# Kernel optimization log

Measured on AMD Instinct MI355X. Metric: run time of the kernel, lower is better.

## Reference

```python
import jax, jax.numpy as jnp
import numpy as np

NU, NI, E = 20000, 8000, 64
DV, DT = 4096, 768
NE, B = 200000, 4096
L_HET, L_HOMO = 2, 1
K_ISG, K_UCG = 10, 20
MMW, WD = 0.1, 1e-4


def setup_inputs() -> dict:
    ks = jax.random.split(jax.random.key(0), 14)
    return {
        "feat_v": jax.random.normal(ks[0], (NI, DV), jnp.float32),
        "feat_t": jax.random.normal(ks[1], (NI, DT), jnp.float32),
        "pref_v": jax.random.normal(ks[2], (NU, E), jnp.float32) * 0.1,
        "pref_t": jax.random.normal(ks[3], (NU, E), jnp.float32) * 0.1,
        "W_v": jax.random.normal(ks[4], (DV, E), jnp.float32) * 0.02,
        "W_t": jax.random.normal(ks[5], (DT, E), jnp.float32) * 0.02,
        "user_v_alpha": jax.random.normal(ks[6], (1,), jnp.float32),
        "user_nb_weights": jax.random.normal(ks[7], (NU, K_UCG), jnp.float32),
        "edge_users": jax.random.randint(ks[8], (NE,), 0, NU, jnp.int32),
        "edge_items": jax.random.randint(ks[9], (NE,), 0, NI, jnp.int32),
        "u_ids": jax.random.randint(ks[10], (B,), 0, NU, jnp.int32),
        "pos_ids": jax.random.randint(ks[11], (B,), 0, NI, jnp.int32),
        "neg_ids": jax.random.randint(ks[12], (B,), 0, NI, jnp.int32),
        "user_nb": jax.random.randint(ks[13], (NU, K_UCG), 0, NU, jnp.int32),
    }


def reference(feat_v, feat_t, pref_v, pref_t, W_v, W_t, user_v_alpha,
              user_nb_weights, edge_users, edge_items, u_ids, pos_ids,
              neg_ids, user_nb):
    N = NU + NI
    # bidirectional bipartite edges (items offset by NU)
    src = jnp.concatenate([edge_users, edge_items + NU])
    dst = jnp.concatenate([edge_items + NU, edge_users])
    deg = jax.ops.segment_sum(jnp.ones_like(src, jnp.float32), dst, num_segments=N)
    deg = jnp.maximum(deg, 1.0)
    norm = (1.0 / jnp.sqrt(deg[src] * deg[dst]))[:, None]

    def hetero_gcn(feat, pref, W):
        x = jnp.concatenate([pref, feat @ W], axis=0)  # [N, E]
        h, out = x, x
        for _ in range(L_HET):
            h = jax.ops.segment_sum(h[src] * norm, dst, num_segments=N)
            out = out + h
        return out[:NU], out[NU:]

    u_v, i_v = hetero_gcn(feat_v, pref_v, W_v)
    u_t, i_t = hetero_gcn(feat_t, pref_t, W_t)
    a_v = jax.nn.sigmoid(user_v_alpha[0])
    u_f = jnp.concatenate([a_v * u_v, (1.0 - a_v) * u_t], axis=1)  # [NU, 2E]
    i_f = jnp.concatenate([i_v, i_t], axis=1)                      # [NI, 2E]

    # Item Semantic Graph: KNN over cosine sim, no grad through adjacency.
    def knn_adj(f):
        fn = f / jnp.linalg.norm(f, axis=-1, keepdims=True)
        sim = fn @ fn.T                       # [NI, NI]
        _, idx = jax.lax.top_k(sim, K_ISG)
        return jnp.zeros((NI, NI), f.dtype).at[jnp.arange(NI)[:, None], idx].set(1.0)

    adj = jax.lax.stop_gradient(MMW * knn_adj(feat_v) + (1.0 - MMW) * knn_adj(feat_t))
    rs = adj.sum(axis=1)
    adj = adj * jnp.where(rs > 0, 1.0 / rs, 0.0)[:, None]

    h_i = i_f
    for _ in range(L_HOMO):
        h_i = adj @ h_i

    # User Co-occurrence Graph: scatter-softmax attention aggregation, vectorized.
    attn = jax.nn.softmax(user_nb_weights, axis=1)  # [NU, K]
    h_u = u_f
    for _ in range(L_HOMO):
        h_u = jnp.einsum('uk,ukd->ud', attn, h_u[user_nb])

    z_u = u_f + h_u
    z_i = i_f + h_i
    pos = jnp.sum(z_u[u_ids] * z_i[pos_ids], axis=1)
    neg = jnp.sum(z_u[u_ids] * z_i[neg_ids], axis=1)
    bpr = -jnp.mean(jax.nn.log_sigmoid(pos - neg))
    reg = WD * (jnp.sum(pref_v ** 2) + jnp.sum(pref_t ** 2) + user_v_alpha[0] ** 2) / 2.0
    return bpr + reg
```

## Files before the change

kernel.cpp:

```cpp
#include <hip/hip_runtime.h>
#include <cstdint>
#include <cstddef>

#define NU_C   20000
#define NI_C   8000
#define NTOT_C 28000
#define NE_C   200000
#define B_C    4096
#define NPAD_C 8064
#define NCHUNK 63
#define NPAIR  2016

typedef unsigned short u16;
typedef unsigned int   u32;
typedef unsigned char  u8;
typedef __bf16 bf16x8 __attribute__((ext_vector_type(8)));
typedef float  f32x4  __attribute__((ext_vector_type(4)));

static __device__ __forceinline__ u16 f2bf(float f) {
  u32 u = __float_as_uint(f);
  return (u16)((u + 0x7fffu + ((u >> 16) & 1u)) >> 16);
}

static __device__ __forceinline__ void gl_lds16(const void* g, void* l) {
  __builtin_amdgcn_global_load_lds(
      (const __attribute__((address_space(1))) void*)g,
      (__attribute__((address_space(3))) void*)l, 16, 0, 0);
}

static __device__ __forceinline__ int xcd_swz(int b) {
  return (b & 7) * (NPAIR / 8) + (b >> 3);
}

static __device__ __forceinline__ void wtrans_body(int b, const float* __restrict__ Wv,
                                                   const float* __restrict__ Wti,
                                                   u16* __restrict__ Ov, u16* __restrict__ Ot) {
  __shared__ u16 sT[64][72];
  const float* W; u16* O; int D;
  if (b < 64) { W = Wv; O = Ov; D = 4096; }
  else        { b -= 64; W = Wti; O = Ot; D = 768; }
  const int k0 = b * 64;
  const int r = threadIdx.x >> 6;
  const int c = threadIdx.x & 63;
  for (int rr = r; rr < 64; rr += 4)
    sT[c][rr] = f2bf(W[(size_t)(k0 + rr) * 64 + c]);
  __syncthreads();
  const int n = threadIdx.x >> 2, seg = threadIdx.x & 3;
  uint4 a0 = *(const uint4*)&sT[n][seg * 16];
  uint4 a1 = *(const uint4*)&sT[n][seg * 16 + 8];
  *(uint4*)(O + (size_t)n * D + k0 + seg * 16)     = a0;
  *(uint4*)(O + (size_t)n * D + k0 + seg * 16 + 8) = a1;
}

__global__ void conv_kernel2(const float* __restrict__ Fv, const float* __restrict__ Ft,
                             u16* __restrict__ Fbv, u16* __restrict__ Fbt,
                             u8* __restrict__ Fv8,
                             float* __restrict__ rnv, float* __restrict__ rnt,
                             const float* __restrict__ pv, const float* __restrict__ pt,
                             float* __restrict__ x2,
                             const float* __restrict__ Wv, const float* __restrict__ Wti,
                             u16* __restrict__ wtv, u16* __restrict__ wtt,
                             const int* __restrict__ eu, const int* __restrict__ ei,
                             float* __restrict__ deg) {
  int b = blockIdx.x;
  const int tid = threadIdx.x;
  float ss = 0.f;
  if (b < NPAD_C) {
    const int row = b;
    u16* dst  = Fbv + (size_t)row * 4096;
    u8*  dst8 = Fv8 + (size_t)row * 4096;
    if (row < NI_C) {
      const float* src = Fv + (size_t)row * 4096;
      for (int c = tid * 4; c < 4096; c += 1024) {
        float4 f = *(const float4*)(src + c);
        ss += f.x*f.x + f.y*f.y + f.z*f.z + f.w*f.w;
        ushort4 v; v.x = f2bf(f.x); v.y = f2bf(f.y); v.z = f2bf(f.z); v.w = f2bf(f.w);
        *(ushort4*)(dst + c) = v;
        int w8 = __builtin_amdgcn_cvt_pk_fp8_f32(f.x, f.y, 0, false);
        w8 = __builtin_amdgcn_cvt_pk_fp8_f32(f.z, f.w, w8, true);
        *(u32*)(dst8 + c) = (u32)w8;
      }
    } else {
      for (int c = tid * 4; c < 4096; c += 1024) {
        ushort4 v; v.x = v.y = v.z = v.w = 0;
        *(ushort4*)(dst + c) = v;
        *(u32*)(dst8 + c) = 0u;
      }
    }
    #pragma unroll
    for (int off = 32; off; off >>= 1) ss += __shfl_xor(ss, off);
    __shared__ float red[4];
    if ((tid & 63) == 0) red[tid >> 6] = ss;
    __syncthreads();
    if (tid == 0) {
      float s = red[0] + red[1] + red[2] + red[3];
      rnv[row] = (row < NI_C) ? rsqrtf(s) : 0.f;
    }
  } else if (b < 2 * NPAD_C) {
    const int row = b - NPAD_C;
    u16* dst = Fbt + (size_t)row * 768;
    if (row < NI_C) {
      const float* src = Ft + (size_t)row * 768;
      for (int c = tid * 4; c < 768; c += 1024) {
        float4 f = *(const float4*)(src + c);
        ss += f.x*f.x + f.y*f.y + f.z*f.z + f.w*f.w;
        ushort4 v; v.x = f2bf(f.x); v.y = f2bf(f.y); v.z = f2bf(f.z); v.w = f2bf(f.w);
        *(ushort4*)(dst + c) = v;
      }
    } else {
      for (int c = tid * 4; c < 768; c += 1024) {
        ushort4 v; v.x = v.y = v.z = v.w = 0;
        *(ushort4*)(dst + c) = v;
      }
    }
    #pragma unroll
    for (int off = 32; off; off >>= 1) ss += __shfl_xor(ss, off);
    __shared__ float red[4];
    if ((tid & 63) == 0) red[tid >> 6] = ss;
    __syncthreads();
    if (tid == 0) {
      float s = red[0] + red[1] + red[2] + red[3];
      rnt[row] = (row < NI_C) ? rsqrtf(s) : 0.f;
    }
  } else if (b < 2 * NPAD_C + 76) {
    wtrans_body(b - 2 * NPAD_C, Wv, Wti, wtv, wtt);
  } else if (b < 2 * NPAD_C + 76 + 1250) {
    const int b2 = b - (2 * NPAD_C + 76);
    #pragma unroll
    for (int k = 0; k < 8; ++k) {
      int gid = b2 * 2048 + k * 256 + tid;
      int u = gid >> 7, c = gid & 127;
      x2[gid] = (c < 64) ? pv[(size_t)u * 64 + c] : pt[(size_t)u * 64 + (c - 64)];
    }
  } else {
    const int b2 = b - (2 * NPAD_C + 76 + 1250);
    int e = b2 * 256 + tid;
    if (e < NE_C) {
      atomicAdd(&deg[eu[e]], 1.f);
      atomicAdd(&deg[NU_C + ei[e]], 1.f);
    }
  }
}

static __device__ __forceinline__ void simtopk_fp8_body(
    int bid, char* smem, const u8* __restrict__ F, const float* __restrict__ rn,
    u32* __restrict__ tv) {
  u8*    sB   = (u8*)smem;
  u8*    sA   = (u8*)(smem + 16384);
  float* T    = (float*)smem;
  int*   mk   = (int*)smem;
  int*   mk2  = (int*)(smem + 20480);
  float* sRNI = (float*)(smem + 33792);
  float* sRNJ = (float*)(smem + 34304);

  const int tid  = threadIdx.x;
  const int lane = tid & 63;
  const int wv   = tid >> 6;
  const int n15  = lane & 15;
  const int quad = lane >> 4;

  int I = 0, rem = xcd_swz(bid);
  { int rowlen = NCHUNK;
    while (rem >= rowlen) { rem -= rowlen; rowlen--; I++; } }
  const int J = I + rem;

  const int l2   = lane >> 2;
  const int lseg = (lane & 3) ^ (l2 & 3) ^ (lane >> 4);
  const u8* gB[2]; const u8* gA[2]; u8* lB[2]; u8* lA[2];
  #pragma unroll
  for (int rep = 0; rep < 2; ++rep) {
    int row = wv * 32 + rep * 16 + l2;
    gB[rep] = F + (size_t)(I * 128 + row) * 4096 + lseg * 16;
    gA[rep] = F + (size_t)(J * 128 + row) * 4096 + lseg * 16;
    lB[rep] = sB + (wv * 32 + rep * 16) * 64;
    lA[rep] = sA + (wv * 32 + rep * 16) * 64;
  }
  const int s_n = (n15 & 3) ^ (n15 >> 2);
  const int q2  = quad >> 1;
  const int q8  = (quad & 1) * 8;
  const int rB0 = (wv * 32 + n15) * 64;
  const int rB1 = rB0 + 16 * 64;

  f32x4 acc[2][8];
  #pragma unroll
  for (int tf = 0; tf < 2; ++tf)
    #pragma unroll
    for (int af = 0; af < 8; ++af) { f32x4 z = {0.f,0.f,0.f,0.f}; acc[tf][af] = z; }

  for (int k0 = 0; k0 < 4096; k0 += 128) {
    __syncthreads();
    gl_lds16(gB[0] + k0,      lB[0]);
    gl_lds16(gB[0] + k0 + 64, lB[0] + 8192);
    gl_lds16(gB[1] + k0,      lB[1]);
    gl_lds16(gB[1] + k0 + 64, lB[1] + 8192);
    gl_lds16(gA[0] + k0,      lA[0]);
    gl_lds16(gA[0] + k0 + 64, lA[0] + 8192);
    gl_lds16(gA[1] + k0,      lA[1]);
    gl_lds16(gA[1] + k0 + 64, lA[1] + 8192);
    if (k0 == 0) {
      if (tid < 128) sRNJ[tid] = rn[J * 128 + tid];
      else           sRNI[tid - 128] = rn[I * 128 + (tid - 128)];
    }
    __syncthreads();
    #pragma unroll
    for (int ksub = 0; ksub < 2; ++ksub) {
      const u8* bBase = sB + ksub * 8192;
      const u8* aBase = sA + ksub * 8192;
      #pragma unroll
      for (int ks = 0; ks < 2; ++ks) {
        const int sw = (((ks * 2 + q2) ^ s_n) << 4) + q8;
        long long b0 = *(const long long*)(bBase + rB0 + sw);
        long long b1 = *(const long long*)(bBase + rB1 + sw);
        #pragma unroll
        for (int af = 0; af < 8; ++af) {
          long long a = *(const long long*)(aBase + (af * 16 + n15) * 64 + sw);
          acc[0][af] = __builtin_amdgcn_mfma_f32_16x16x32_fp8_fp8(a, b0, acc[0][af], 0, 0, 0);
          acc[1][af] = __builtin_amdgcn_mfma_f32_16x16x32_fp8_fp8(a, b1, acc[1][af], 0, 0, 0);
        }
      }
    }
  }

  int bk[2][10];
  #pragma unroll
  for (int tf = 0; tf < 2; ++tf)
    #pragma unroll
    for (int j = 0; j < 10; ++j) bk[tf][j] = 0;

  #pragma unroll
  for (int af = 0; af < 8; ++af) {
    const float4 rn4 = *(const float4*)(sRNJ + af * 16 + quad * 4);
    const float rna[4] = {rn4.x, rn4.y, rn4.z, rn4.w};
    #pragma unroll
    for (int r = 0; r < 4; ++r) {
      const int ci = J * 128 + af * 16 + quad * 4 + r;
      #pragma unroll
      for (int tf = 0; tf < 2; ++tf) {
        float v = acc[tf][af][r] * rna[r];
        int key = (int)((__float_as_uint(v) & 0xFFFFE000u) | (u32)ci);
        if (ci < NI_C && key > bk[tf][9]) {
          bk[tf][9] = key;
          #pragma unroll
          for (int j = 9; j > 0; --j)
            if (bk[tf][j] > bk[tf][j-1]) { int t = bk[tf][j]; bk[tf][j] = bk[tf][j-1]; bk[tf][j-1] = t; }
        }
      }
    }
  }
  __syncthreads();
  #pragma unroll
  for (int tf = 0; tf < 2; ++tf) {
    int rl = wv * 32 + tf * 16 + n15;
    #pragma unroll
    for (int j = 0; j < 10; ++j) mk[rl * 40 + quad * 10 + j] = bk[tf][j];
  }
  __syncthreads();
  if (tid < 128) {
    int* m = mk + tid * 40;
    int h0 = 0, h1 = 10, h2 = 20, h3 = 30;
    int v0 = m[0], v1 = m[10], v2 = m[20], v3 = m[30];
    #pragma unroll
    for (int s = 0; s < 10; ++s) {
      int m01 = v0 > v1 ? v0 : v1, m23 = v2 > v3 ? v2 : v3;
      int mx = m01 > m23 ? m01 : m23;
      mk2[tid * 10 + s] = mx;
      if      (mx == v0) { ++h0; v0 = (h0 < 10) ? m[h0] : (int)0x80000000; }
      else if (mx == v1) { ++h1; v1 = (h1 < 20) ? m[h1] : (int)0x80000000; }
      else if (mx == v2) { ++h2; v2 = (h2 < 30) ? m[h2] : (int)0x80000000; }
      else               { ++h3; v3 = (h3 < 40) ? m[h3] : (int)0x80000000; }
    }
  }
  __syncthreads();
  { u32* o = tv + ((size_t)J * NPAD_C + I * 128) * 10;
    for (int g = tid; g < 1280; g += 256) o[g] = (u32)mk2[g]; }

  if (I == J) return;

  int bj[2][10];
  #pragma unroll
  for (int s = 0; s < 2; ++s)
    #pragma unroll
    for (int j = 0; j < 10; ++j) bj[s][j] = 0;

  #pragma unroll
  for (int tf = 0; tf < 2; ++tf) {
    __syncthreads();
    #pragma unroll
    for (int af = 0; af < 8; ++af)
      #pragma unroll
      for (int r = 0; r < 4; ++r)
        T[(af * 16 + quad * 4 + r) * 66 + wv * 16 + n15] = acc[tf][af][r];
    __syncthreads();
    #pragma unroll
    for (int s = 0; s < 2; ++s) {
      const int c_own = wv * 32 + s * 16 + n15;
      #pragma unroll
      for (int j = 0; j < 16; ++j) {
        const int t  = quad * 32 + tf * 16 + j;
        const int t64 = quad * 16 + j;
        float v = T[c_own * 66 + t64] * sRNI[t];
        const int ti = I * 128 + t;
        int key = (int)((__float_as_uint(v) & 0xFFFFE000u) | (u32)ti);
        if (ti < NI_C && key > bj[s][9]) {
          bj[s][9] = key;
          #pragma unroll
          for (int q = 9; q > 0; --q)
            if (bj[s][q] > bj[s][q-1]) { int tt = bj[s][q]; bj[s][q] = bj[s][q-1]; bj[s][q-1] = tt; }
        }
      }
    }
  }
  __syncthreads();
  #pragma unroll
  for (int s = 0; s < 2; ++s) {
    int rl = wv * 32 + s * 16 + n15;
    #pragma unroll
    for (int j = 0; j < 10; ++j) mk[rl * 40 + quad * 10 + j] = bj[s][j];
  }
  __syncthreads();
  if (tid < 128) {
    int* m = mk + tid * 40;
    int h0 = 0, h1 = 10, h2 = 20, h3 = 30;
    int v0 = m[0], v1 = m[10], v2 = m[20], v3 = m[30];
    #pragma unroll
    for (int s = 0; s < 10; ++s) {
      int m01 = v0 > v1 ? v0 : v1, m23 = v2 > v3 ? v2 : v3;
      int mx = m01 > m23 ? m01 : m23;
      mk2[tid * 10 + s] = mx;
      if      (mx == v0) { ++h0; v0 = (h0 < 10) ? m[h0] : (int)0x80000000; }
      else if (mx == v1) { ++h1; v1 = (h1 < 20) ? m[h1] : (int)0x80000000; }
      else if (mx == v2) { ++h2; v2 = (h2 < 30) ? m[h2] : (int)0x80000000; }
      else               { ++h3; v3 = (h3 < 40) ? m[h3] : (int)0x80000000; }
    }
  }
  __syncthreads();
  { u32* o = tv + ((size_t)I * NPAD_C + J * 128) * 10;
    for (int g = tid; g < 1280; g += 256) o[g] = (u32)mk2[g]; }
}

static __device__ __forceinline__ void simtopk_bf16_body(
    int bid, char* smem, const u16* __restrict__ F, const float* __restrict__ rn,
    u32* __restrict__ tv) {
  u16*   sB   = (u16*)smem;
  u16*   sA   = (u16*)(smem + 16384);
  float* T    = (float*)smem;
  int*   mk   = (int*)smem;
  int*   mk2  = (int*)(smem + 20480);
  float* sRNI = (float*)(smem + 34816);
  float* sRNJ = (float*)(smem + 35328);

  const int tid  = threadIdx.x;
  const int lane = tid & 63;
  const int wv   = tid >> 6;
  const int n15  = lane & 15;
  const int quad = lane >> 4;

  int I = 0, rem = xcd_swz(bid);
  { int rowlen = NCHUNK;
    while (rem >= rowlen) { rem -= rowlen; rowlen--; I++; } }
  const int J = I + rem;

  const int l8  = lane >> 3;
  const int sgu = ((lane & 7) ^ l8) << 3;
  const u16* gB[4]; const u16* gA[4]; u16* lB[4]; u16* lA[4];
  #pragma unroll
  for (int rep = 0; rep < 4; ++rep) {
    int row = wv * 32 + rep * 8 + l8;
    gB[rep] = F + (size_t)(I * 128 + row) * 768 + sgu;
    gA[rep] = F + (size_t)(J * 128 + row) * 768 + sgu;
    lB[rep] = sB + wv * 2048 + rep * 512;
    lA[rep] = sA + wv * 2048 + rep * 512;
  }
  const int swu0 = ((quad    ) ^ (n15 & 7)) << 3;
  const int swu1 = ((quad + 4) ^ (n15 & 7)) << 3;
  const int rowB0 = (wv * 32 + n15) * 64;
  const int rowB1 = rowB0 + 16 * 64;

  f32x4 acc[2][8];
  #pragma unroll
  for (int tf = 0; tf < 2; ++tf)
    #pragma unroll
    for (int af = 0; af < 8; ++af) { f32x4 z = {0.f,0.f,0.f,0.f}; acc[tf][af] = z; }

  for (int k0 = 0; k0 < 768; k0 += 64) {
    __syncthreads();
    #pragma unroll
    for (int rep = 0; rep < 4; ++rep) gl_lds16(gB[rep] + k0, lB[rep]);
    #pragma unroll
    for (int rep = 0; rep < 4; ++rep) gl_lds16(gA[rep] + k0, lA[rep]);
    if (k0 == 0) {
      if (tid < 128) sRNJ[tid] = rn[J * 128 + tid];
      else           sRNI[tid - 128] = rn[I * 128 + (tid - 128)];
    }
    __syncthreads();
    #pragma unroll
    for (int ks = 0; ks < 2; ++ks) {
      const int swu = ks ? swu1 : swu0;
      bf16x8 b0 = *(const bf16x8*)(sB + rowB0 + swu);
      bf16x8 b1 = *(const bf16x8*)(sB + rowB1 + swu);
      #pragma unroll
      for (int af = 0; af < 8; ++af) {
        bf16x8 a = *(const bf16x8*)(sA + (af * 16 + n15) * 64 + swu);
        acc[0][af] = __builtin_amdgcn_mfma_f32_16x16x32_bf16(a, b0, acc[0][af], 0, 0, 0);
        acc[1][af] = __builtin_amdgcn_mfma_f32_16x16x32_bf16(a, b1, acc[1][af], 0, 0, 0);
      }
    }
  }

  int bk[2][10];
  #pragma unroll
  for (int tf = 0; tf < 2; ++tf)
    #pragma unroll
    for (int j = 0; j < 10; ++j) bk[tf][j] = 0;

  #pragma unroll
  for (int af = 0; af < 8; ++af) {
    const float4 rn4 = *(const float4*)(sRNJ + af * 16 + quad * 4);
    const float rna[4] = {rn4.x, rn4.y, rn4.z, rn4.w};
    #pragma unroll
    for (int r = 0; r < 4; ++r) {
      const int ci = J * 128 + af * 16 + quad * 4 + r;
      #pragma unroll
      for (int tf = 0; tf < 2; ++tf) {
        float v = acc[tf][af][r] * rna[r];
        int key = (int)((__float_as_uint(v) & 0xFFFFE000u) | (u32)ci);
        if (ci < NI_C && key > bk[tf][9]) {
          bk[tf][9] = key;
          #pragma unroll
          for (int j = 9; j > 0; --j)
            if (bk[tf][j] > bk[tf][j-1]) { int t = bk[tf][j]; bk[tf][j] = bk[tf][j-1]; bk[tf][j-1] = t; }
        }
      }
    }
  }
  __syncthreads();
  #pragma unroll
  for (int tf = 0; tf < 2; ++tf) {
    int rl = wv * 32 + tf * 16 + n15;
    #pragma unroll
    for (int j = 0; j < 10; ++j) mk[rl * 40 + quad * 10 + j] = bk[tf][j];
  }
  __syncthreads();
  if (tid < 128) {
    int* m = mk + tid * 40;
    int h0 = 0, h1 = 10, h2 = 20, h3 = 30;
    int v0 = m[0], v1 = m[10], v2 = m[20], v3 = m[30];
    #pragma unroll
    for (int s = 0; s < 10; ++s) {
      int m01 = v0 > v1 ? v0 : v1, m23 = v2 > v3 ? v2 : v3;
      int mx = m01 > m23 ? m01 : m23;
      mk2[tid * 10 + s] = mx;
      if      (mx == v0) { ++h0; v0 = (h0 < 10) ? m[h0] : (int)0x80000000; }
      else if (mx == v1) { ++h1; v1 = (h1 < 20) ? m[h1] : (int)0x80000000; }
      else if (mx == v2) { ++h2; v2 = (h2 < 30) ? m[h2] : (int)0x80000000; }
      else               { ++h3; v3 = (h3 < 40) ? m[h3] : (int)0x80000000; }
    }
  }
  __syncthreads();
  { u32* o = tv + ((size_t)J * NPAD_C + I * 128) * 10;
    for (int g = tid; g < 1280; g += 256) o[g] = (u32)mk2[g]; }

  if (I == J) return;

  int bj[2][10];
  #pragma unroll
  for (int s = 0; s < 2; ++s)
    #pragma unroll
    for (int j = 0; j < 10; ++j) bj[s][j] = 0;

  #pragma unroll
  for (int tf = 0; tf < 2; ++tf) {
    __syncthreads();
    #pragma unroll
    for (int af = 0; af < 8; ++af)
      #pragma unroll
      for (int r = 0; r < 4; ++r)
        T[(af * 16 + quad * 4 + r) * 66 + wv * 16 + n15] = acc[tf][af][r];
    __syncthreads();
    #pragma unroll
    for (int s = 0; s < 2; ++s) {
      const int c_own = wv * 32 + s * 16 + n15;
      #pragma unroll
      for (int j = 0; j < 16; ++j) {
        const int t  = quad * 32 + tf * 16 + j;
        const int t64 = quad * 16 + j;
        float v = T[c_own * 66 + t64] * sRNI[t];
        const int ti = I * 128 + t;
        int key = (int)((__float_as_uint(v) & 0xFFFFE000u) | (u32)ti);
        if (ti < NI_C && key > bj[s][9]) {
          bj[s][9] = key;
          #pragma unroll
          for (int q = 9; q > 0; --q)
            if (bj[s][q] > bj[s][q-1]) { int tt = bj[s][q]; bj[s][q] = bj[s][q-1]; bj[s][q-1] = tt; }
        }
      }
    }
  }
  __syncthreads();
  #pragma unroll
  for (int s = 0; s < 2; ++s) {
    int rl = wv * 32 + s * 16 + n15;
    #pragma unroll
    for (int j = 0; j < 10; ++j) mk[rl * 40 + quad * 10 + j] = bj[s][j];
  }
  __syncthreads();
  if (tid < 128) {
    int* m = mk + tid * 40;
    int h0 = 0, h1 = 10, h2 = 20, h3 = 30;
    int v0 = m[0], v1 = m[10], v2 = m[20], v3 = m[30];
    #pragma unroll
    for (int s = 0; s < 10; ++s) {
      int m01 = v0 > v1 ? v0 : v1, m23 = v2 > v3 ? v2 : v3;
      int mx = m01 > m23 ? m01 : m23;
      mk2[tid * 10 + s] = mx;
      if      (mx == v0) { ++h0; v0 = (h0 < 10) ? m[h0] : (int)0x80000000; }
      else if (mx == v1) { ++h1; v1 = (h1 < 20) ? m[h1] : (int)0x80000000; }
      else if (mx == v2) { ++h2; v2 = (h2 < 30) ? m[h2] : (int)0x80000000; }
      else               { ++h3; v3 = (h3 < 40) ? m[h3] : (int)0x80000000; }
    }
  }
  __syncthreads();
  { u32* o = tv + ((size_t)I * NPAD_C + J * 128) * 10;
    for (int g = tid; g < 1280; g += 256) o[g] = (u32)mk2[g]; }
}

static __device__ __forceinline__ void merge4_body(int mb, int* fkbase,
                                                   const u32* __restrict__ tv,
                                                   int* __restrict__ idx) {
  const int w    = threadIdx.x >> 6;
  const int lane = threadIdx.x & 63;
  const int row  = mb * 4 + w;
  int* fk = fkbase + w * 640;
  for (int g = lane; g < 630; g += 64)
    fk[g] = (int)tv[((size_t)(g / 10) * NPAD_C + row) * 10 + (g % 10)];
  if (lane < 10) fk[630 + lane] = (int)0x80000000;
  __syncthreads();
  int v[10];
  #pragma unroll
  for (int j = 0; j < 10; ++j) v[j] = fk[lane + j * 64];
  #pragma unroll 1
  for (int s = 0; s < 10; ++s) {
    int loc = v[0];
    #pragma unroll
    for (int j = 1; j < 10; ++j) loc = v[j] > loc ? v[j] : loc;
    #pragma unroll
    for (int off = 32; off; off >>= 1) {
      int o = __shfl_xor(loc, off); loc = o > loc ? o : loc;
    }
    if (lane == 0) idx[row * 10 + s] = loc & 0x1FFF;
    #pragma unroll
    for (int j = 0; j < 10; ++j) if (v[j] == loc) v[j] = (int)0x80000000;
  }
}

template<int D>
static __device__ __forceinline__ void gemm_xw_body(
    int bid, char* smem, const u16* __restrict__ F, const u16* __restrict__ Wt,
    float* __restrict__ x2, int modeoff) {
  u16* sF = (u16*)smem;
  const int tid  = threadIdx.x;
  const int lane = tid & 63;
  const int wv   = tid >> 6;
  const int n15  = lane & 15;
  const int quad = lane >> 4;
  const int l8   = lane >> 3;
  const int sgu  = ((lane & 7) ^ l8) << 3;
  const u16* gF[2]; u16* lF[2];
  #pragma unroll
  for (int rep = 0; rep < 2; ++rep) {
    int row = rep * 32 + wv * 8 + l8;
    gF[rep] = F + (size_t)(bid * 64 + row) * D + sgu;
    lF[rep] = sF + (rep * 32 + wv * 8) * 64;
  }
  const int swu0 = ((quad    ) ^ (n15 & 7)) << 3;
  const int swu1 = ((quad + 4) ^ (n15 & 7)) << 3;

  f32x4 acc[4];
  #pragma unroll
  for (int nf = 0; nf < 4; ++nf) { f32x4 z = {0.f,0.f,0.f,0.f}; acc[nf] = z; }

  for (int k0 = 0; k0 < D; k0 += 64) {
    __syncthreads();
    gl_lds16(gF[0] + k0, lF[0]);
    gl_lds16(gF[1] + k0, lF[1]);
    __syncthreads();
    #pragma unroll
    for (int ks = 0; ks < 2; ++ks) {
      const int swu = ks ? swu1 : swu0;
      bf16x8 a = *(const bf16x8*)(sF + (wv * 16 + n15) * 64 + swu);
      #pragma unroll
      for (int nf = 0; nf < 4; ++nf) {
        bf16x8 b = *(const bf16x8*)(Wt + (size_t)(nf * 16 + n15) * D + k0 + ks * 32 + quad * 8);
        acc[nf] = __builtin_amdgcn_mfma_f32_16x16x32_bf16(a, b, acc[nf], 0, 0, 0);
      }
    }
  }
  #pragma unroll
  for (int nf = 0; nf < 4; ++nf)
    #pragma unroll
    for (int r = 0; r < 4; ++r) {
      int row = bid * 64 + wv * 16 + quad * 4 + r;
      if (row < NI_C)
        x2[(size_t)(NU_C + row) * 128 + modeoff + nf * 16 + n15] = acc[nf][r];
    }
}

static __device__ __forceinline__ void gather2_body(
    int bid, const int* __restrict__ row_start, const int* __restrict__ esrc,
    const float* __restrict__ ew, const float* __restrict__ x2, float* __restrict__ h1) {
  const int node = bid * 2 + (threadIdx.x >> 7);
  const int ch   = threadIdx.x & 127;
  if (node >= NTOT_C) return;
  const int b = row_start[node], e = row_start[node + 1];
  float acc = 0.f;
  for (int i = b; i < e; ++i)
    acc += ew[i] * x2[(size_t)esrc[i] * 128 + ch];
  h1[(size_t)node * 128 + ch] = acc;
}

static __device__ __forceinline__ void gather_comb2_body(
    int bid, const int* __restrict__ row_start, const int* __restrict__ esrc,
    const float* __restrict__ ew, const float* __restrict__ x2,
    const float* __restrict__ h1, const float* __restrict__ alpha,
    float* __restrict__ uf, float* __restrict__ ifb) {
  const int node = bid * 2 + (threadIdx.x >> 7);
  const int ch   = threadIdx.x & 127;
  if (node >= NTOT_C) return;
  const int b = row_start[node], e = row_start[node + 1];
  float acc = 0.f;
  for (int i = b; i < e; ++i)
    acc += ew[i] * h1[(size_t)esrc[i] * 128 + ch];
  float val = x2[(size_t)node * 128 + ch] + h1[(size_t)node * 128 + ch] + acc;
  if (node < NU_C) {
    float av = 1.f / (1.f + expf(-alpha[0]));
    float coef = (ch < 64) ? av : (1.f - av);
    uf[(size_t)node * 128 + ch] = coef * val;
  } else {
    ifb[(size_t)(node - NU_C) * 128 + ch] = val;
  }
}

static __device__ __forceinline__ void place_body(
    int bid, const int* __restrict__ eu, const int* __restrict__ ei,
    const float* __restrict__ dinv, int* __restrict__ cursor,
    int* __restrict__ esrc, float* __restrict__ ew) {
  int e = bid * 256 + threadIdx.x;
  if (e >= NE_C) return;
  int u = eu[e], v = NU_C + ei[e];
  float w = dinv[u] * dinv[v];
  int p1 = atomicAdd(&cursor[v], 1);  esrc[p1] = u; ew[p1] = w;
  int p2 = atomicAdd(&cursor[u], 1);  esrc[p2] = v; ew[p2] = w;
}

__launch_bounds__(256)
__global__ void fusedA_kernel(const u8* __restrict__ F8, const float* __restrict__ rnv,
                              u32* __restrict__ tv,
                              const u16* __restrict__ Fvb, const u16* __restrict__ Wtv,
                              const u16* __restrict__ Ftb, const u16* __restrict__ Wtt,
                              float* __restrict__ x2,
                              const int* __restrict__ eu, const int* __restrict__ ei,
                              const float* __restrict__ dinv, int* __restrict__ cursor,
                              int* __restrict__ esrc, float* __restrict__ ew) {
  __shared__ __align__(16) char smem[34816];
  int b = blockIdx.x;
  if (b < 125) { gemm_xw_body<4096>(b, smem, Fvb, Wtv, x2, 0); return; }
  b -= 125;
  if (b < 125) { gemm_xw_body<768>(b, smem, Ftb, Wtt, x2, 64); return; }
  b -= 125;
  if (b < NPAIR) { simtopk_fp8_body(b, smem, F8, rnv, tv); return; }
  place_body(b - NPAIR, eu, ei, dinv, cursor, esrc, ew);
}

__launch_bounds__(256)
__global__ void fusedB_kernel(const u16* __restrict__ Ftb, const float* __restrict__ rnt,
                              u32* __restrict__ tv2,
                              const u32* __restrict__ tv, int* __restrict__ idx,
                              const int* __restrict__ row_start, const int* __restrict__ esrc,
                              const float* __restrict__ ew, const float* __restrict__ x2,
                              float* __restrict__ h1) {
  __shared__ __align__(16) char smem[40960];
  int b = blockIdx.x;
  if (b < NPAIR) { simtopk_bf16_body(b, smem, Ftb, rnt, tv2); return; }
  b -= NPAIR;
  if (b < 2000) { merge4_body(b, (int*)smem, tv, idx); return; }
  gather2_body(b - 2000, row_start, esrc, ew, x2, h1);
}

__launch_bounds__(256)
__global__ void fusedC_kernel(const u32* __restrict__ tv2, int* __restrict__ idxt,
                              const int* __restrict__ row_start, const int* __restrict__ esrc,
                              const float* __restrict__ ew, const float* __restrict__ x2,
                              const float* __restrict__ h1, const float* __restrict__ alpha,
                              float* __restrict__ uf, float* __restrict__ ifb) {
  __shared__ __align__(16) int fk[4 * 640];
  int b = blockIdx.x;
  if (b < 2000) { merge4_body(b, fk, tv2, idxt); return; }
  gather_comb2_body(b - 2000, row_start, esrc, ew, x2, h1, alpha, uf, ifb);
}

__global__ void scan_kernel(float* __restrict__ deg, int* __restrict__ row_start,
                            int* __restrict__ cursor) {
  __shared__ int part[1024];
  const int tid = threadIdx.x;
  const int base = tid * 28;
  float dl[28];
  int local[28];
  int s = 0;
  #pragma unroll
  for (int j = 0; j < 28; ++j) {
    int n = base + j;
    float df = (n < NTOT_C) ? deg[n] : 0.f;
    dl[j] = df;
    local[j] = s; s += (int)df;
  }
  part[tid] = s;
  __syncthreads();
  for (int off = 1; off < 1024; off <<= 1) {
    int v = (tid >= off) ? part[tid - off] : 0;
    __syncthreads();
    part[tid] += v;
    __syncthreads();
  }
  int pre = (tid > 0) ? part[tid - 1] : 0;
  #pragma unroll
  for (int j = 0; j < 28; ++j) {
    int n = base + j;
    if (n < NTOT_C) {
      row_start[n] = pre + local[j];
      cursor[n]    = pre + local[j];
      deg[n]       = rsqrtf(fmaxf(dl[j], 1.f));
    }
  }
  if (tid == 1023) row_start[NTOT_C] = part[1023];
}

__global__ void zuzi_kernel(const float* __restrict__ uf, const float* __restrict__ w,
                            const int* __restrict__ nb, const float* __restrict__ ifb,
                            const int* __restrict__ iv, const int* __restrict__ it,
                            float* __restrict__ zu, float* __restrict__ zi) {
  const int c = threadIdx.x;
  if (blockIdx.x < NU_C) {
    const int u = blockIdx.x;
    __shared__ float at[20];
    if (c < 20) at[c] = w[u * 20 + c];
    __syncthreads();
    float e[20]; float m = -1e30f;
    #pragma unroll
    for (int k = 0; k < 20; ++k) { e[k] = at[k]; m = fmaxf(m, e[k]); }
    float ssum = 0.f;
    #pragma unroll
    for (int k = 0; k < 20; ++k) { e[k] = expf(e[k] - m); ssum += e[k]; }
    float inv = 1.f / ssum;
    float acc = 0.f;
    #pragma unroll
    for (int k = 0; k < 20; ++k) {
      int j = nb[u * 20 + k];
      acc += e[k] * inv * uf[(size_t)j * 128 + c];
    }
    zu[(size_t)u * 128 + c] = uf[(size_t)u * 128 + c] + acc;
  } else {
    const int i = blockIdx.x - NU_C;
    float sv = 0.f, st = 0.f;
    #pragma unroll
    for (int k = 0; k < 10; ++k) sv += ifb[(size_t)iv[i * 10 + k] * 128 + c];
    #pragma unroll
    for (int k = 0; k < 10; ++k) st += ifb[(size_t)it[i * 10 + k] * 128 + c];
    zi[(size_t)i * 128 + c] = ifb[(size_t)i * 128 + c] + 0.01f * sv + 0.09f * st;
  }
}

__global__ void loss_kernel(const float* __restrict__ zu, const float* __restrict__ zi,
                            const int* __restrict__ uid, const int* __restrict__ pid,
                            const int* __restrict__ nid, const float* __restrict__ pv,
                            const float* __restrict__ pt, const float* __restrict__ alpha,
                            float* __restrict__ out) {
  if (blockIdx.x < 1024) {
    int wv = threadIdx.x >> 6, lane = threadIdx.x & 63;
    int b = blockIdx.x * 4 + wv;
    int u = uid[b], p = pid[b], n = nid[b];
    float2 a  = *(const float2*)(zu + (size_t)u * 128 + lane * 2);
    float2 xp = *(const float2*)(zi + (size_t)p * 128 + lane * 2);
    float2 xn = *(const float2*)(zi + (size_t)n * 128 + lane * 2);
    float d = a.x * (xp.x - xn.x) + a.y * (xp.y - xn.y);
    #pragma unroll
    for (int off = 32; off; off >>= 1) d += __shfl_xor(d, off);
    if (lane == 0) {
      float xv = -d;
      float sp = fmaxf(xv, 0.f) + log1pf(expf(-fabsf(xv)));
      atomicAdd(out, sp * (1.f / (float)B_C));
    }
  } else {
    const size_t N1 = (size_t)NU_C * 64;
    float acc = 0.f;
    for (size_t i = (size_t)(blockIdx.x - 1024) * 256 + threadIdx.x; i < 2 * N1;
         i += (size_t)512 * 256) {
      float x = (i < N1) ? pv[i] : pt[i - N1];
      acc += x * x;
    }
    #pragma unroll
    for (int off = 32; off; off >>= 1) acc += __shfl_xor(acc, off);
    __shared__ float red[4];
    if ((threadIdx.x & 63) == 0) red[threadIdx.x >> 6] = acc;
    __syncthreads();
    if (threadIdx.x == 0) {
      float s = red[0] + red[1] + red[2] + red[3];
      atomicAdd(out, 0.5e-4f * s);
    }
    if (blockIdx.x == 1024 && threadIdx.x == 0) {
      float a = alpha[0];
      atomicAdd(out, 0.5e-4f * a * a);
    }
  }
}

extern "C" void kernel_launch(void* const* d_in, const int* in_sizes, int n_in,
                              void* d_out, int out_size, void* d_ws, size_t ws_size,
                              hipStream_t stream) {
  const float* feat_v = (const float*)d_in[0];
  const float* feat_t = (const float*)d_in[1];
  const float* pref_v = (const float*)d_in[2];
  const float* pref_t = (const float*)d_in[3];
  const float* W_v    = (const float*)d_in[4];
  const float* W_t    = (const float*)d_in[5];
  const float* alpha  = (const float*)d_in[6];
  const float* unw    = (const float*)d_in[7];
  const int* eu       = (const int*)d_in[8];
  const int* ei       = (const int*)d_in[9];
  const int* u_ids    = (const int*)d_in[10];
  const int* pos_ids  = (const int*)d_in[11];
  const int* neg_ids  = (const int*)d_in[12];
  const int* user_nb  = (const int*)d_in[13];
  float* out = (float*)d_out;
  char* ws = (char*)d_ws;

  size_t off = 0;
  auto alloc = [&](size_t bytes) { char* p = ws + off; off += (bytes + 255) & ~(size_t)255; return p; };
  u16*   fvbf  = (u16*)alloc((size_t)NPAD_C * 4096 * 2);
  u8*    fv8   = (u8*)alloc((size_t)NPAD_C * 4096);
  u16*   ftbf  = (u16*)alloc((size_t)NPAD_C * 768 * 2);
  u16*   wtv   = (u16*)alloc((size_t)64 * 4096 * 2);
  u16*   wtt   = (u16*)alloc((size_t)64 * 768 * 2);
  float* rn_v  = (float*)alloc(NPAD_C * 4);
  float* rn_t  = (float*)alloc(NPAD_C * 4);
  int*   idx_v = (int*)alloc(NI_C * 10 * 4);
  int*   idx_t = (int*)alloc(NI_C * 10 * 4);
  float* dinv  = (float*)alloc(NTOT_C * 4);
  int*   rowst = (int*)alloc((NTOT_C + 1) * 4);
  int*   curs  = (int*)alloc(NTOT_C * 4);
  int*   esrc  = (int*)alloc((size_t)2 * NE_C * 4);
  float* ew    = (float*)alloc((size_t)2 * NE_C * 4);
  float* x2    = (float*)alloc((size_t)NTOT_C * 128 * 4);
  float* h1    = (float*)alloc((size_t)NTOT_C * 128 * 4);
  char*  pC    = alloc((size_t)(NU_C + NI_C) * 128 * 4 * 2);
  u32*   tvb   = (u32*)pC;
  u32*   tvb2  = (u32*)fvbf;
  float* u_f   = (float*)pC;
  float* i_f   = (float*)(pC + (size_t)NU_C * 128 * 4);
  float* z_u   = (float*)(pC + (size_t)(NU_C + NI_C) * 128 * 4);
  float* z_i   = (float*)(pC + (size_t)(2 * NU_C + NI_C) * 128 * 4);

  hipMemsetAsync(out, 0, sizeof(float), stream);
  hipMemsetAsync(dinv, 0, NTOT_C * 4, stream);

  conv_kernel2<<<2 * NPAD_C + 76 + 1250 + (NE_C + 255) / 256, 256, 0, stream>>>(
      feat_v, feat_t, fvbf, ftbf, fv8, rn_v, rn_t, pref_v, pref_t, x2,
      W_v, W_t, wtv, wtt, eu, ei, dinv);

  scan_kernel<<<1, 1024, 0, stream>>>(dinv, rowst, curs);

  fusedA_kernel<<<250 + NPAIR + (NE_C + 255) / 256, 256, 0, stream>>>(
      fv8, rn_v, tvb, fvbf, wtv, ftbf, wtt, x2, eu, ei, dinv, curs, esrc, ew);

  fusedB_kernel<<<NPAIR + 2000 + 14000, 256, 0, stream>>>(
      ftbf, rn_t, tvb2, tvb, idx_v, rowst, esrc, ew, x2, h1);

  fusedC_kernel<<<2000 + 14000, 256, 0, stream>>>(
      tvb2, idx_t, rowst, esrc, ew, x2, h1, alpha, u_f, i_f);

  zuzi_kernel<<<NU_C + NI_C, 128, 0, stream>>>(u_f, unw, user_nb, i_f, idx_v, idx_t, z_u, z_i);
  loss_kernel<<<1536, 256, 0, stream>>>(z_u, z_i, u_ids, pos_ids, neg_ids,
                                        pref_v, pref_t, alpha, out);
}
```

Baseline: 1.004 ms.

## Compute z_u/z_i only for sampled batch rows fused into loss kernel

```diff
diff --git a/kernel.cpp b/kernel.cpp
--- a/kernel.cpp
+++ b/kernel.cpp
@@ -10,6 +10,7 @@
 #define NPAD_C 8064
 #define NCHUNK 63
 #define NPAIR  2016
+#define NEB    782
 
 typedef unsigned short u16;
 typedef unsigned int   u32;
@@ -61,7 +62,8 @@
                              const float* __restrict__ Wv, const float* __restrict__ Wti,
                              u16* __restrict__ wtv, u16* __restrict__ wtt,
                              const int* __restrict__ eu, const int* __restrict__ ei,
-                             float* __restrict__ deg) {
+                             float* __restrict__ deg,
+                             const float* __restrict__ alpha, float* __restrict__ out) {
   int b = blockIdx.x;
   const int tid = threadIdx.x;
   float ss = 0.f;
@@ -132,12 +134,33 @@
       int u = gid >> 7, c = gid & 127;
       x2[gid] = (c < 64) ? pv[(size_t)u * 64 + c] : pt[(size_t)u * 64 + (c - 64)];
     }
-  } else {
+  } else if (b < 2 * NPAD_C + 76 + 1250 + NEB) {
     const int b2 = b - (2 * NPAD_C + 76 + 1250);
     int e = b2 * 256 + tid;
     if (e < NE_C) {
       atomicAdd(&deg[eu[e]], 1.f);
       atomicAdd(&deg[NU_C + ei[e]], 1.f);
+    }
+  } else {
+    const int b2 = b - (2 * NPAD_C + 76 + 1250 + NEB);
+    const size_t N1 = (size_t)NU_C * 64;
+    float acc = 0.f;
+    for (size_t i = (size_t)b2 * 256 + tid; i < 2 * N1; i += (size_t)512 * 256) {
+      float x = (i < N1) ? pv[i] : pt[i - N1];
+      acc += x * x;
+    }
+    #pragma unroll
+    for (int off = 32; off; off >>= 1) acc += __shfl_xor(acc, off);
+    __shared__ float red2[4];
+    if ((tid & 63) == 0) red2[tid >> 6] = acc;
+    __syncthreads();
+    if (tid == 0) {
+      float s = red2[0] + red2[1] + red2[2] + red2[3];
+      atomicAdd(out, 0.5e-4f * s);
+    }
+    if (b2 == 0 && tid == 0) {
+      float a = alpha[0];
+      atomicAdd(out, 0.5e-4f * a * a);
     }
   }
 }
@@ -734,82 +757,65 @@
   if (tid == 1023) row_start[NTOT_C] = part[1023];
 }
 
-__global__ void zuzi_kernel(const float* __restrict__ uf, const float* __restrict__ w,
-                            const int* __restrict__ nb, const float* __restrict__ ifb,
-                            const int* __restrict__ iv, const int* __restrict__ it,
-                            float* __restrict__ zu, float* __restrict__ zi) {
-  const int c = threadIdx.x;
-  if (blockIdx.x < NU_C) {
-    const int u = blockIdx.x;
-    __shared__ float at[20];
-    if (c < 20) at[c] = w[u * 20 + c];
-    __syncthreads();
-    float e[20]; float m = -1e30f;
-    #pragma unroll
-    for (int k = 0; k < 20; ++k) { e[k] = at[k]; m = fmaxf(m, e[k]); }
-    float ssum = 0.f;
-    #pragma unroll
-    for (int k = 0; k < 20; ++k) { e[k] = expf(e[k] - m); ssum += e[k]; }
-    float inv = 1.f / ssum;
-    float acc = 0.f;
-    #pragma unroll
-    for (int k = 0; k < 20; ++k) {
-      int j = nb[u * 20 + k];
-      acc += e[k] * inv * uf[(size_t)j * 128 + c];
-    }
-    zu[(size_t)u * 128 + c] = uf[(size_t)u * 128 + c] + acc;
-  } else {
-    const int i = blockIdx.x - NU_C;
-    float sv = 0.f, st = 0.f;
-    #pragma unroll
-    for (int k = 0; k < 10; ++k) sv += ifb[(size_t)iv[i * 10 + k] * 128 + c];
-    #pragma unroll
-    for (int k = 0; k < 10; ++k) st += ifb[(size_t)it[i * 10 + k] * 128 + c];
-    zi[(size_t)i * 128 + c] = ifb[(size_t)i * 128 + c] + 0.01f * sv + 0.09f * st;
-  }
-}
-
-__global__ void loss_kernel(const float* __restrict__ zu, const float* __restrict__ zi,
-                            const int* __restrict__ uid, const int* __restrict__ pid,
-                            const int* __restrict__ nid, const float* __restrict__ pv,
-                            const float* __restrict__ pt, const float* __restrict__ alpha,
-                            float* __restrict__ out) {
-  if (blockIdx.x < 1024) {
-    int wv = threadIdx.x >> 6, lane = threadIdx.x & 63;
-    int b = blockIdx.x * 4 + wv;
-    int u = uid[b], p = pid[b], n = nid[b];
-    float2 a  = *(const float2*)(zu + (size_t)u * 128 + lane * 2);
-    float2 xp = *(const float2*)(zi + (size_t)p * 128 + lane * 2);
-    float2 xn = *(const float2*)(zi + (size_t)n * 128 + lane * 2);
-    float d = a.x * (xp.x - xn.x) + a.y * (xp.y - xn.y);
-    #pragma unroll
-    for (int off = 32; off; off >>= 1) d += __shfl_xor(d, off);
-    if (lane == 0) {
-      float xv = -d;
-      float sp = fmaxf(xv, 0.f) + log1pf(expf(-fabsf(xv)));
-      atomicAdd(out, sp * (1.f / (float)B_C));
-    }
-  } else {
-    const size_t N1 = (size_t)NU_C * 64;
-    float acc = 0.f;
-    for (size_t i = (size_t)(blockIdx.x - 1024) * 256 + threadIdx.x; i < 2 * N1;
-         i += (size_t)512 * 256) {
-      float x = (i < N1) ? pv[i] : pt[i - N1];
-      acc += x * x;
-    }
-    #pragma unroll
-    for (int off = 32; off; off >>= 1) acc += __shfl_xor(acc, off);
-    __shared__ float red[4];
-    if ((threadIdx.x & 63) == 0) red[threadIdx.x >> 6] = acc;
-    __syncthreads();
-    if (threadIdx.x == 0) {
-      float s = red[0] + red[1] + red[2] + red[3];
-      atomicAdd(out, 0.5e-4f * s);
-    }
-    if (blockIdx.x == 1024 && threadIdx.x == 0) {
-      float a = alpha[0];
-      atomicAdd(out, 0.5e-4f * a * a);
-    }
+__launch_bounds__(256)
+__global__ void zuloss_kernel(const float* __restrict__ uf, const float* __restrict__ w,
+                              const int* __restrict__ nb, const float* __restrict__ ifb,
+                              const int* __restrict__ iv, const int* __restrict__ it,
+                              const int* __restrict__ uid, const int* __restrict__ pid,
+                              const int* __restrict__ nid, float* __restrict__ out) {
+  const int wv = threadIdx.x >> 6, lane = threadIdx.x & 63;
+  const int b = blockIdx.x * 4 + wv;
+  const int u = uid[b], p = pid[b], n = nid[b];
+  const int c = lane * 2;
+
+  float e[20]; float m = -1e30f;
+  #pragma unroll
+  for (int k = 0; k < 20; ++k) { e[k] = w[u * 20 + k]; m = fmaxf(m, e[k]); }
+  float ssum = 0.f;
+  #pragma unroll
+  for (int k = 0; k < 20; ++k) { e[k] = expf(e[k] - m); ssum += e[k]; }
+  float inv = 1.f / ssum;
+
+  float2 zu = *(const float2*)(uf + (size_t)u * 128 + c);
+  float ax = 0.f, ay = 0.f;
+  #pragma unroll
+  for (int k = 0; k < 20; ++k) {
+    int j = nb[u * 20 + k];
+    float2 t = *(const float2*)(uf + (size_t)j * 128 + c);
+    ax += e[k] * inv * t.x;
+    ay += e[k] * inv * t.y;
+  }
+  zu.x += ax; zu.y += ay;
+
+  float2 zp, zn;
+  #pragma unroll
+  for (int side = 0; side < 2; ++side) {
+    const int i = side ? n : p;
+    float svx = 0.f, svy = 0.f, stx = 0.f, sty = 0.f;
+    #pragma unroll
+    for (int k = 0; k < 10; ++k) {
+      float2 t = *(const float2*)(ifb + (size_t)iv[i * 10 + k] * 128 + c);
+      svx += t.x; svy += t.y;
+    }
+    #pragma unroll
+    for (int k = 0; k < 10; ++k) {
+      float2 t = *(const float2*)(ifb + (size_t)it[i * 10 + k] * 128 + c);
+      stx += t.x; sty += t.y;
+    }
+    float2 base = *(const float2*)(ifb + (size_t)i * 128 + c);
+    float2 r;
+    r.x = base.x + 0.01f * svx + 0.09f * stx;
+    r.y = base.y + 0.01f * svy + 0.09f * sty;
+    if (side) zn = r; else zp = r;
+  }
+
+  float d = zu.x * (zp.x - zn.x) + zu.y * (zp.y - zn.y);
+  #pragma unroll
+  for (int off = 32; off; off >>= 1) d += __shfl_xor(d, off);
+  if (lane == 0) {
+    float xv = -d;
+    float sp = fmaxf(xv, 0.f) + log1pf(expf(-fabsf(xv)));
+    atomicAdd(out, sp * (1.f / (float)B_C));
   }
 }
 
@@ -851,24 +857,24 @@
   float* ew    = (float*)alloc((size_t)2 * NE_C * 4);
   float* x2    = (float*)alloc((size_t)NTOT_C * 128 * 4);
   float* h1    = (float*)alloc((size_t)NTOT_C * 128 * 4);
-  char*  pC    = alloc((size_t)(NU_C + NI_C) * 128 * 4 * 2);
+  char*  pC    = alloc((size_t)(NU_C + NI_C) * 128 * 4);
   u32*   tvb   = (u32*)pC;
+  char*  pC2   = alloc((size_t)6 * 1024 * 1024 + 256);
+  (void)pC2;
   u32*   tvb2  = (u32*)fvbf;
   float* u_f   = (float*)pC;
   float* i_f   = (float*)(pC + (size_t)NU_C * 128 * 4);
-  float* z_u   = (float*)(pC + (size_t)(NU_C + NI_C) * 128 * 4);
-  float* z_i   = (float*)(pC + (size_t)(2 * NU_C + NI_C) * 128 * 4);
 
   hipMemsetAsync(out, 0, sizeof(float), stream);
   hipMemsetAsync(dinv, 0, NTOT_C * 4, stream);
 
-  conv_kernel2<<<2 * NPAD_C + 76 + 1250 + (NE_C + 255) / 256, 256, 0, stream>>>(
+  conv_kernel2<<<2 * NPAD_C + 76 + 1250 + NEB + 512, 256, 0, stream>>>(
       feat_v, feat_t, fvbf, ftbf, fv8, rn_v, rn_t, pref_v, pref_t, x2,
-      W_v, W_t, wtv, wtt, eu, ei, dinv);
+      W_v, W_t, wtv, wtt, eu, ei, dinv, alpha, out);
 
   scan_kernel<<<1, 1024, 0, stream>>>(dinv, rowst, curs);
 
-  fusedA_kernel<<<250 + NPAIR + (NE_C + 255) / 256, 256, 0, stream>>>(
+  fusedA_kernel<<<250 + NPAIR + NEB, 256, 0, stream>>>(
       fv8, rn_v, tvb, fvbf, wtv, ftbf, wtt, x2, eu, ei, dinv, curs, esrc, ew);
 
   fusedB_kernel<<<NPAIR + 2000 + 14000, 256, 0, stream>>>(
@@ -877,7 +883,6 @@
   fusedC_kernel<<<2000 + 14000, 256, 0, stream>>>(
       tvb2, idx_t, rowst, esrc, ew, x2, h1, alpha, u_f, i_f);
 
-  zuzi_kernel<<<NU_C + NI_C, 128, 0, stream>>>(u_f, unw, user_nb, i_f, idx_v, idx_t, z_u, z_i);
-  loss_kernel<<<1536, 256, 0, stream>>>(z_u, z_i, u_ids, pos_ids, neg_ids,
-                                        pref_v, pref_t, alpha, out);
-}
+  zuloss_kernel<<<1024, 256, 0, stream>>>(u_f, unw, user_nb, i_f, idx_v, idx_t,
+                                          u_ids, pos_ids, neg_ids, out);
+}
```

Measured after the change: 986.0 us. About the same (-1.8%).
